# Performance work log

Hardware: AMD Instinct MI355X
Metric: run time of the kernel (lower is better)

The kernel has to match this reference:

```python
import jax, jax.numpy as jnp
import numpy as np

NQ, NT, D = 8192, 8192, 128
EC, EQ, ET = 262144, 262144, 262144


def seg_softmax(logits, seg, num):
    # numerically stable segment softmax over a 1-D logits vector
    m = jax.ops.segment_max(logits, seg, num_segments=num)
    e = jnp.exp(logits - m[seg])
    s = jax.ops.segment_sum(e, seg, num_segments=num)
    return e / s[seg]


def _linear_params(key, din, dout):
    k1, k2 = jax.random.split(key)
    scale = 1.0 / np.sqrt(din)
    W = jax.random.uniform(k1, (din, dout), minval=-scale, maxval=scale, dtype=jnp.float32)
    b = jax.random.uniform(k2, (dout,), minval=-scale, maxval=scale, dtype=jnp.float32)
    return W, b


def setup_inputs():
    key = jax.random.key(0)
    ks = jax.random.split(key, 20)
    inp = {
        'Xq': jax.random.normal(ks[0], (NQ, D), dtype=jnp.float32),
        'edge_index_q': jax.random.randint(ks[1], (2, EQ), 0, NQ),
        'Xt': jax.random.normal(ks[2], (NT, D), dtype=jnp.float32),
        'edge_index_t': jax.random.randint(ks[3], (2, ET), 0, NT),
        'norm_q': jax.random.uniform(ks[4], (NQ, 1), dtype=jnp.float32),
        'norm_t': jax.random.uniform(ks[5], (NT, 1), dtype=jnp.float32),
        'cross_src': jax.random.randint(ks[6], (EC,), 0, NQ),
        'cross_dst': jax.random.randint(ks[7], (EC,), 0, NT),
        'node_mask': jnp.ones((NQ,), dtype=bool),
        'only_run_inter': 0,
    }
    names_dims = [
        ('ac_q', D, D), ('ac_t', D, D), ('vc_q', D, D), ('vc_t', D, D),
        ('mq', 2 * D, D), ('mt', 3 * D, D),
        ('aq', 2 * D, 1), ('vq', 2 * D, D), ('at', 2 * D, 1), ('vt', 2 * D, D),
    ]
    for i, (nm, din, dout) in enumerate(names_dims):
        W, b = _linear_params(ks[8 + i], din, dout)
        inp['W_' + nm] = W
        inp['b_' + nm] = b
    return inp


def reference(Xq, edge_index_q, Xt, edge_index_t, norm_q, norm_t, cross_src, cross_dst,
              node_mask, only_run_inter,
              W_ac_q, b_ac_q, W_ac_t, b_ac_t, W_vc_q, b_vc_q, W_vc_t, b_vc_t,
              W_mq, b_mq, W_mt, b_mt,
              W_aq, b_aq, W_vq, b_vq, W_at, b_at, W_vt, b_vt):
    elu = jax.nn.elu
    nq, nt, d = Xq.shape[0], Xt.shape[0], Xq.shape[1]

    # cross-graph attention logits: per (u, v) pair, dot of transformed features
    Xq_ac = elu(Xq @ W_ac_q + b_ac_q)
    Xt_ac = elu(Xt @ W_ac_t + b_ac_t)
    att_logits = jnp.sum(Xq_ac[cross_src] * Xt_ac[cross_dst], axis=-1)  # [EC]

    # t2q: aggregate target values into query nodes (faithful to original: values gathered by u indices)
    Xt_vc = elu(Xt @ W_vc_t + b_vc_t)
    att_u = seg_softmax(att_logits, cross_src, nq)[:, None]
    Xt2q = jax.ops.segment_sum(att_u * Xt_vc[cross_src], cross_src, num_segments=nq)
    Xq_merged = jnp.concatenate([Xq, Xt2q], axis=1) @ W_mq + b_mq

    # q2t: aggregate query values into target nodes, plus global query summary Q
    Xq_vc = elu(Xq @ W_vc_q + b_vc_q)
    att_v = seg_softmax(att_logits, cross_dst, nt)[:, None]
    Xq2t = jax.ops.segment_sum(att_v * Xq_vc[cross_src], cross_dst, num_segments=nt)
    Q = jnp.broadcast_to(jnp.mean(Xq, axis=0, keepdims=True), (nt, d))
    Xt_merged = jnp.concatenate([Xt, Xq2t, Q], axis=1) @ W_mt + b_mt

    if only_run_inter:
        return Xq_merged, Xt_merged

    # intra-graph edge-wise gather -> MLP -> softmax-scatter message passing
    msg_t = jnp.concatenate([Xt_merged[edge_index_t[0]], Xt_merged[edge_index_t[1]]], axis=1)  # [ET, 2D]
    a_t = seg_softmax((msg_t @ W_at + b_at)[:, 0], edge_index_t[1], nt)[:, None]
    Xt_out = jax.ops.segment_sum(a_t * (msg_t @ W_vt + b_vt), edge_index_t[1], num_segments=nt)

    msg_q = jnp.concatenate([Xq_merged[edge_index_q[0]], Xq_merged[edge_index_q[1]]], axis=1)  # [EQ, 2D]
    a_q = seg_softmax((msg_q @ W_aq + b_aq)[:, 0], edge_index_q[1], nq)[:, None]
    Xq_out = jax.ops.segment_sum(a_q * (msg_q @ W_vq + b_vq), edge_index_q[1], num_segments=nq)

    return Xq_out, Xt_out
```

## Files before the change

### kernel.cpp

```cpp
#include <hip/hip_runtime.h>
#include <math.h>


#define NBIN 8192
#define NB   128

typedef _Float16 h2f __attribute__((ext_vector_type(2)));
typedef __attribute__((ext_vector_type(8))) short short8;
typedef __attribute__((ext_vector_type(4))) float f32x4;

__device__ __forceinline__ float elu1(float x) { return x > 0.f ? x : __expf(x) - 1.f; }

__device__ __forceinline__ unsigned short f2bf(float x) {
    unsigned u = __float_as_uint(x);
    u += 0x7FFF + ((u >> 16) & 1);
    return (unsigned short)(u >> 16);
}
__device__ __forceinline__ float bflo(unsigned u) { return __uint_as_float(u << 16); }
__device__ __forceinline__ float bfhi(unsigned u) { return __uint_as_float(u & 0xFFFF0000u); }
__device__ __forceinline__ unsigned short f2h(float x) {
    return __builtin_bit_cast(unsigned short, (_Float16)x);
}

__device__ __forceinline__ float dot8_f16(const uint4 a, const uint4 b, float d) {
#if __has_builtin(__builtin_amdgcn_fdot2)
    d = __builtin_amdgcn_fdot2(__builtin_bit_cast(h2f, a.x), __builtin_bit_cast(h2f, b.x), d, false);
    d = __builtin_amdgcn_fdot2(__builtin_bit_cast(h2f, a.y), __builtin_bit_cast(h2f, b.y), d, false);
    d = __builtin_amdgcn_fdot2(__builtin_bit_cast(h2f, a.z), __builtin_bit_cast(h2f, b.z), d, false);
    d = __builtin_amdgcn_fdot2(__builtin_bit_cast(h2f, a.w), __builtin_bit_cast(h2f, b.w), d, false);
#else
    const unsigned ua[4] = { a.x, a.y, a.z, a.w };
    const unsigned ub[4] = { b.x, b.y, b.z, b.w };
    #pragma unroll
    for (int t = 0; t < 4; ++t) {
        const h2f ha = __builtin_bit_cast(h2f, ua[t]);
        const h2f hb = __builtin_bit_cast(h2f, ub[t]);
        d = fmaf((float)ha.x, (float)hb.x, d);
        d = fmaf((float)ha.y, (float)hb.y, d);
    }
#endif
    return d;
}

__device__ void wprep_body(const float* __restrict__ S, unsigned short* __restrict__ Wf)
{
    const int lane = threadIdx.x & 63;
    const int fg = threadIdx.x >> 6;
    const int l15 = lane & 15, quad = lane >> 4;
    for (int f = fg; f < 32; f += 4) {
        const int nt = f >> 2, kc = f & 3;
        const int n = nt * 16 + l15;
        const int ks = kc * 32 + quad * 8;
        unsigned short pk[8];
        #pragma unroll
        for (int jj = 0; jj < 8; ++jj)
            pk[jj] = f2bf(S[(size_t)(ks + jj) * 128 + n]);
        uint4 v;
        v.x = (unsigned)pk[0] | ((unsigned)pk[1] << 16);
        v.y = (unsigned)pk[2] | ((unsigned)pk[3] << 16);
        v.z = (unsigned)pk[4] | ((unsigned)pk[5] << 16);
        v.w = (unsigned)pk[6] | ((unsigned)pk[7] << 16);
        *(uint4*)&Wf[((size_t)f * 64 + lane) * 8] = v;
    }
}

__device__ void hist_body(int k, int a, int* h,
                          const int* __restrict__ cs, const int* __restrict__ cd,
                          const int* __restrict__ et1, const int* __restrict__ eq1,
                          int* __restrict__ mask_src, unsigned short* __restrict__ partial,
                          int EC, int ET, int EQ)
{
    const int tid = threadIdx.x;
    const int* idxs[3] = { cd, et1, eq1 };
    const int Es[3] = { EC, ET, EQ };
    for (int b = tid; b < NBIN; b += 256) h[b] = 0;
    __syncthreads();
    const int E = Es[a];
    const int per = (E + NB - 1) / NB;
    const int lo = k * per;
    const int hi = min(E, lo + per);
    const int* idx = idxs[a];
    for (int e = lo + tid; e < hi; e += 256) {
        atomicAdd(&h[idx[e]], 1);
        if (a == 0) mask_src[cs[e]] = 1;
    }
    __syncthreads();
    unsigned short* P = partial + ((size_t)a * NB + k) * NBIN;
    for (int b = tid; b < NBIN; b += 256) P[b] = (unsigned short)h[b];
}

__device__ void colsum_body(int bx, const float* __restrict__ X, float* __restrict__ sum)
{
    const int c = threadIdx.x & 127;
    const int half = threadIdx.x >> 7;
    float s = 0.f;
    #pragma unroll 8
    for (int j = 0; j < 64; ++j) {
        const int r = bx * 128 + half + 2 * j;
        s += X[(size_t)r * 128 + c];
    }
    atomicAdd(&sum[c], s);
}

struct WSrcs { const float* s[12]; };

__global__ __launch_bounds__(256) void prep(
    const int* cs, const int* cd, const int* et1, const int* eq1,
    int* mask_src, unsigned short* partial, int EC, int ET, int EQ,
    WSrcs ws, unsigned short* wt, const float* Xq, float* Qsum)
{
    __shared__ int smem_h[NBIN];
    int b = blockIdx.x;
    if (b < 3 * NB) {
        hist_body(b % NB, b / NB, smem_h, cs, cd, et1, eq1, mask_src, partial, EC, ET, EQ);
    } else if ((b -= 3 * NB) < 12) {
        wprep_body(ws.s[b], wt + (size_t)b * 16384);
    } else {
        colsum_body(b - 12, Xq, Qsum);
    }
}

struct MJob {
    const float* A0; const float* A1; const int* rowmask1;
    const unsigned short* W[2][2];
    const float* bias0; const float* bias1;
    float* C0; float* C1;
    unsigned short* Cb0; unsigned short* Cb1;
    unsigned short* Ch0; unsigned short* Ch1;
    const float* gvw; float* gvo;
    int act;
};

__global__ __launch_bounds__(256) void gemm_mfma(MJob j0, MJob j1)
{
    const MJob j = blockIdx.z ? j1 : j0;
    const int c0 = blockIdx.y * 64;
    const int r0 = blockIdx.x * 64;
    __shared__ unsigned short AhL[64][136];
    __shared__ unsigned short AlL[64][136];
    const int tid = threadIdx.x;
    const int wv = tid >> 6, lane = tid & 63;
    const int l15 = lane & 15, quad = lane >> 4;

    f32x4 acc[2][4] = {};

    for (int pass = 0; pass < 2; ++pass) {
        const float* A = pass ? j.A1 : j.A0;
        if (!A) break;
        {
            const int row = tid >> 2, kq = (tid & 3) * 32;
            const int gr = r0 + row;
            const bool zero = pass && j.rowmask1 && (j.rowmask1[gr] == 0);
            const float* src = A + (size_t)gr * 128 + kq;
            #pragma unroll
            for (int c = 0; c < 32; c += 4) {
                float4 v = *(const float4*)(src + c);
                if (zero) v = make_float4(0.f, 0.f, 0.f, 0.f);
                const float xv[4] = { v.x, v.y, v.z, v.w };
                unsigned short hh[4], ll[4];
                #pragma unroll
                for (int u = 0; u < 4; ++u) {
                    const unsigned short hb = f2bf(xv[u]);
                    hh[u] = hb;
                    ll[u] = f2bf(xv[u] - __uint_as_float((unsigned)hb << 16));
                }
                uint2 ph, pl;
                ph.x = (unsigned)hh[0] | ((unsigned)hh[1] << 16);
                ph.y = (unsigned)hh[2] | ((unsigned)hh[3] << 16);
                pl.x = (unsigned)ll[0] | ((unsigned)ll[1] << 16);
                pl.y = (unsigned)ll[2] | ((unsigned)ll[3] << 16);
                *(uint2*)&AhL[row][kq + c] = ph;
                *(uint2*)&AlL[row][kq + c] = pl;
            }
        }
        __syncthreads();
        #pragma unroll
        for (int kc = 0; kc < 4; ++kc) {
            const short8 ah = *(const short8*)&AhL[wv * 16 + l15][kc * 32 + quad * 8];
            const short8 al = *(const short8*)&AlL[wv * 16 + l15][kc * 32 + quad * 8];
            #pragma unroll
            for (int out = 0; out < 2; ++out) {
                const unsigned short* Wf = j.W[pass][out];
                if (!Wf) continue;
                #pragma unroll
                for (int ni = 0; ni < 4; ++ni) {
                    const short8 bh = *(const short8*)&Wf[
                        ((size_t)(((c0 >> 4) + ni) * 4 + kc) * 64 + lane) * 8];
                    acc[out][ni] = __builtin_amdgcn_mfma_f32_16x16x32_bf16(ah, bh, acc[out][ni], 0, 0, 0);
                    acc[out][ni] = __builtin_amdgcn_mfma_f32_16x16x32_bf16(al, bh, acc[out][ni], 0, 0, 0);
                }
            }
        }
        __syncthreads();
    }

    #pragma unroll
    for (int out = 0; out < 2; ++out) {
        if (!j.W[0][out] && !j.W[1][out]) continue;
        const float* bias = out ? j.bias1 : j.bias0;
        float* C = out ? j.C1 : j.C0;
        unsigned short* Cb = out ? j.Cb1 : j.Cb0;
        unsigned short* Ch = out ? j.Ch1 : j.Ch0;
        const int dogv = (j.gvw != nullptr) && (out == 0);
        float p[4] = {};
        #pragma unroll
        for (int ni = 0; ni < 4; ++ni) {
            const int col = c0 + ni * 16 + l15;
            const float bvl = bias ? bias[col] : 0.f;
            const float gw = dogv ? j.gvw[col] : 0.f;
            #pragma unroll
            for (int reg = 0; reg < 4; ++reg) {
                float o = acc[out][ni][reg] + bvl;
                if (j.act) o = elu1(o);
                const int row = r0 + wv * 16 + quad * 4 + reg;
                if (C) C[(size_t)row * 128 + col] = o;
                else if (Cb) Cb[(size_t)row * 128 + col] = f2bf(o);
                else Ch[(size_t)row * 128 + col] = f2h(o);
                p[reg] = fmaf(o, gw, p[reg]);
            }
        }
        if (dogv) {
            #pragma unroll
            for (int reg = 0; reg < 4; ++reg) {
                float v = p[reg];
                v += __shfl_xor(v, 1, 64); v += __shfl_xor(v, 2, 64);
                v += __shfl_xor(v, 4, 64); v += __shfl_xor(v, 8, 64);
                if (l15 == 0)
                    atomicAdd(j.gvo + r0 + wv * 16 + quad * 4 + reg, v);
            }
        }
    }
}

__global__ void binprefix_kernel(unsigned short* __restrict__ partial, int* __restrict__ cnt)
{
    const int bin = blockIdx.x * 256 + threadIdx.x;
    const int a = blockIdx.y;
    unsigned short* P = partial + (size_t)a * NB * NBIN;
    int s = 0;
    #pragma unroll 4
    for (int k = 0; k < NB; ++k) {
        const int p = P[(size_t)k * NBIN + bin];
        P[(size_t)k * NBIN + bin] = (unsigned short)s;
        s += p;
    }
    cnt[a * NBIN + bin] = s;
}

__global__ __launch_bounds__(1024) void scan3_kernel(const int* __restrict__ cnt, int* __restrict__ offs)
{
    const int b = blockIdx.x;
    const int* c = cnt + (size_t)b * NBIN;
    int* o = offs + (size_t)b * (NBIN + 1);
    __shared__ int sums[1024];
    const int tid = threadIdx.x;
    int loc[8]; int s = 0;
    #pragma unroll
    for (int j = 0; j < 8; ++j) { loc[j] = s; s += c[tid * 8 + j]; }
    sums[tid] = s;
    __syncthreads();
    for (int off = 1; off < 1024; off <<= 1) {
        int v = 0;
        if (tid >= off) v = sums[tid - off];
        __syncthreads();
        sums[tid] += v;
        __syncthreads();
    }
    const int ex = tid ? sums[tid - 1] : 0;
    #pragma unroll
    for (int j = 0; j < 8; ++j) o[tid * 8 + j] = ex + loc[j];
    if (tid == 1023) o[NBIN] = sums[1023];
}

__device__ void scatter_body(int k, int a, int* cur,
    const int* __restrict__ cs, const int* __restrict__ cd,
    const int* __restrict__ et0, const int* __restrict__ et1,
    const int* __restrict__ eq0, const int* __restrict__ eq1,
    const unsigned short* __restrict__ partial, const int* __restrict__ offs,
    int* __restrict__ ids_cd, int* __restrict__ ids_t, int* __restrict__ ids_q,
    int EC, int ET, int EQ)
{
    const int tid = threadIdx.x;
    const int Es[3] = { EC, ET, EQ };
    const int* seg[3] = { cd, et1, eq1 };
    const int* pay[3] = { cs, et0, eq0 };
    int* dst[3] = { ids_cd, ids_t, ids_q };
    const unsigned short* P = partial + ((size_t)a * NB + k) * NBIN;
    const int* off = offs + (size_t)a * (NBIN + 1);
    for (int b = tid; b < NBIN; b += 256) cur[b] = off[b] + (int)P[b];
    __syncthreads();
    const int E = Es[a];
    const int per = (E + NB - 1) / NB;
    const int lo = k * per;
    const int hi = min(E, lo + per);
    const int* sg = seg[a]; const int* pl = pay[a]; int* dd = dst[a];
    for (int e = lo + tid; e < hi; e += 256) {
        const int pos = atomicAdd(&cur[sg[e]], 1);
        dd[pos] = pl[e];
    }
}

__device__ void mt_extra_body(float* red,
    const float* __restrict__ Qsum, const float* __restrict__ Wmt,
    const float* __restrict__ bmt, float* __restrict__ outv, int M)
{
    const int c = threadIdx.x & 127, h = threadIdx.x >> 7;
    const float inv = 1.0f / (float)M;
    float acc = 0.f;
    #pragma unroll 4
    for (int k = h * 64; k < h * 64 + 64; ++k)
        acc = fmaf(Qsum[k] * inv, Wmt[(size_t)(256 + k) * 128 + c], acc);
    red[h * 128 + c] = acc;
    __syncthreads();
    if (h == 0) outv[c] = bmt[c] + red[c] + red[128 + c];
}

__global__ __launch_bounds__(256) void stage3(
    const int* cs, const int* cd,
    const int* et0, const int* et1, const int* eq0, const int* eq1,
    const unsigned short* partial, const int* offs,
    int* ids_cd, int* ids_t, int* ids_q, int EC, int ET, int EQ,
    const float* Qsum, const float* Wmt, const float* bmt, float* mte, int M)
{
    __shared__ __align__(16) char smem[32768];
    const int b = blockIdx.x;
    if (b < 3 * NB)
        scatter_body(b % NB, b / NB, (int*)smem, cs, cd, et0, et1, eq0, eq1,
                     partial, offs, ids_cd, ids_t, ids_q, EC, ET, EQ);
    else
        mt_extra_body((float*)smem, Qsum, Wmt, bmt, mte, M);
}

__device__ __forceinline__ void gather_chunk_bf(
    const unsigned int* __restrict__ rows, int myid, float wv, int rem,
    int half, int cl, float4& acc)
{
    const int npairs = (rem + 1) >> 1;
    int j = 0;
    for (; j + 4 <= npairs; j += 4) {
        const int e0 = 2 * j + half, e1 = e0 + 2, e2 = e0 + 4, e3 = e0 + 6;
        const int s0 = __shfl(myid, e0, 64); const float w0 = __shfl(wv, e0, 64);
        const int s1 = __shfl(myid, e1, 64); const float w1 = __shfl(wv, e1, 64);
        const int s2 = __shfl(myid, e2, 64); const float w2 = __shfl(wv, e2, 64);
        const int s3 = __shfl(myid, e3, 64); const float w3 = __shfl(wv, e3, 64);
        const uint2 v0 = *(const uint2*)(rows + (size_t)s0 * 64 + cl * 2);
        const uint2 v1 = *(const uint2*)(rows + (size_t)s1 * 64 + cl * 2);
        const uint2 v2 = *(const uint2*)(rows + (size_t)s2 * 64 + cl * 2);
        const uint2 v3 = *(const uint2*)(rows + (size_t)s3 * 64 + cl * 2);
        acc.x = fmaf(w0, bflo(v0.x), acc.x); acc.y = fmaf(w0, bfhi(v0.x), acc.y);
        acc.z = fmaf(w0, bflo(v0.y), acc.z); acc.w = fmaf(w0, bfhi(v0.y), acc.w);
        acc.x = fmaf(w1, bflo(v1.x), acc.x); acc.y = fmaf(w1, bfhi(v1.x), acc.y);
        acc.z = fmaf(w1, bflo(v1.y), acc.z); acc.w = fmaf(w1, bfhi(v1.y), acc.w);
        acc.x = fmaf(w2, bflo(v2.x), acc.x); acc.y = fmaf(w2, bfhi(v2.x), acc.y);
        acc.z = fmaf(w2, bflo(v2.y), acc.z); acc.w = fmaf(w2, bfhi(v2.y), acc.w);
        acc.x = fmaf(w3, bflo(v3.x), acc.x); acc.y = fmaf(w3, bfhi(v3.x), acc.y);
        acc.z = fmaf(w3, bflo(v3.y), acc.z); acc.w = fmaf(w3, bfhi(v3.y), acc.w);
    }
    for (; j < npairs; ++j) {
        const int e = 2 * j + half;
        const int sv = __shfl(myid, e, 64); const float we = __shfl(wv, e, 64);
        const uint2 v = *(const uint2*)(rows + (size_t)sv * 64 + cl * 2);
        acc.x = fmaf(we, bflo(v.x), acc.x); acc.y = fmaf(we, bfhi(v.x), acc.y);
        acc.z = fmaf(we, bflo(v.y), acc.z); acc.w = fmaf(we, bfhi(v.y), acc.w);
    }
}

__global__ __launch_bounds__(256) void seg_agg_intra(
    const int* ot, const int* it, const float* nlt, const unsigned int* rt,
    const float* xt, const float* ebt, float* outt,
    const int* oq, const int* iq, const float* nlq, const unsigned int* rq,
    const float* xq, const float* ebq, float* outq, int nseg)
{
    const int* offs; const int* ids; const float* nl; const unsigned int* rows;
    const float* extra; const float* eb; float* out;
    if (blockIdx.y == 0) { offs = ot; ids = it; nl = nlt; rows = rt; extra = xt; eb = ebt; out = outt; }
    else                 { offs = oq; ids = iq; nl = nlq; rows = rq; extra = xq; eb = ebq; out = outq; }
    const int wid = (int)((blockIdx.x * blockDim.x + threadIdx.x) >> 6);
    const int lane = threadIdx.x & 63;
    if (wid >= nseg) return;
    const int lo = offs[wid], hi = offs[wid + 1];
    if (lo == hi) {
        *(float2*)(out + (size_t)wid * 128 + lane * 2) = make_float2(0.f, 0.f);
        return;
    }
    const int half = lane >> 5, cl = lane & 31;
    float m = -3.4e38f, s = 0.f;
    float4 acc = make_float4(0.f, 0.f, 0.f, 0.f);
    for (int base = lo; base < hi; base += 64) {
        const int rem = min(64, hi - base);
        int myid = 0; float l = -3.4e38f;
        if (lane < rem) { myid = ids[base + lane]; l = nl[myid]; }
        float mc = l;
        #pragma unroll
        for (int t = 32; t; t >>= 1) mc = fmaxf(mc, __shfl_xor(mc, t, 64));
        const float nm = fmaxf(m, mc);
        const float alpha = __expf(m - nm);
        const float wv = (lane < rem) ? __expf(l - nm) : 0.f;
        s = s * alpha + wv;
        acc.x *= alpha; acc.y *= alpha; acc.z *= alpha; acc.w *= alpha;
        m = nm;
        gather_chunk_bf(rows, myid, wv, rem, half, cl, acc);
    }
    #pragma unroll
    for (int t = 32; t; t >>= 1) s += __shfl_xor(s, t, 64);
    acc.x += __shfl_xor(acc.x, 32, 64); acc.y += __shfl_xor(acc.y, 32, 64);
    acc.z += __shfl_xor(acc.z, 32, 64); acc.w += __shfl_xor(acc.w, 32, 64);
    if (half == 0) {
        const float inv = 1.f / s;
        const float4 xv = *(const float4*)(extra + (size_t)wid * 128 + cl * 4);
        const float4 bv = *(const float4*)(eb + cl * 4);
        float4 o;
        o.x = fmaf(acc.x, inv, xv.x + bv.x);
        o.y = fmaf(acc.y, inv, xv.y + bv.y);
        o.z = fmaf(acc.z, inv, xv.z + bv.z);
        o.w = fmaf(acc.w, inv, xv.w + bv.w);
        *(float4*)(out + (size_t)wid * 128 + cl * 4) = o;
    }
}

__global__ __launch_bounds__(256) void seg_agg_cross(
    const int* __restrict__ offs, const int* __restrict__ ids,
    const unsigned int* __restrict__ Aqh, const unsigned int* __restrict__ Ath,
    const unsigned int* __restrict__ Vqb, float* __restrict__ out, int nseg)
{
    __shared__ unsigned int atrowh[4][64];
    const int w = threadIdx.x >> 6;
    const int lane = threadIdx.x & 63;
    const int wid = blockIdx.x * 4 + w;
    if (wid >= nseg) return;
    const int lo = offs[wid], hi = offs[wid + 1];
    if (lo == hi) {
        *(float2*)(out + (size_t)wid * 128 + lane * 2) = make_float2(0.f, 0.f);
        return;
    }
    atrowh[w][lane] = Ath[(size_t)wid * 64 + lane];
    __threadfence_block();

    const int half = lane >> 5, cl = lane & 31;
    float m = -3.4e38f, s = 0.f;
    float4 acc = make_float4(0.f, 0.f, 0.f, 0.f);
    for (int base = lo; base < hi; base += 64) {
        const int rem = min(64, hi - base);
        int myid = 0; float d = -3.4e38f;
        if (lane < rem) {
            myid = ids[base + lane];
            const unsigned int* ar = Aqh + (size_t)myid * 64;
            d = 0.f;
            #pragma unroll
            for (int k = 0; k < 64; k += 4)
                d = dot8_f16(*(const uint4*)(ar + k), *(const uint4*)&atrowh[w][k], d);
        }
        float mc = d;
        #pragma unroll
        for (int t = 32; t; t >>= 1) mc = fmaxf(mc, __shfl_xor(mc, t, 64));
        const float nm = fmaxf(m, mc);
        const float alpha = __expf(m - nm);
        const float wv = (lane < rem) ? __expf(d - nm) : 0.f;
        s = s * alpha + wv;
        acc.x *= alpha; acc.y *= alpha; acc.z *= alpha; acc.w *= alpha;
        m = nm;
        gather_chunk_bf(Vqb, myid, wv, rem, half, cl, acc);
    }
    #pragma unroll
    for (int t = 32; t; t >>= 1) s += __shfl_xor(s, t, 64);
    acc.x += __shfl_xor(acc.x, 32, 64); acc.y += __shfl_xor(acc.y, 32, 64);
    acc.z += __shfl_xor(acc.z, 32, 64); acc.w += __shfl_xor(acc.w, 32, 64);
    if (half == 0) {
        const float inv = 1.f / s;
        float4 o;
        o.x = acc.x * inv; o.y = acc.y * inv; o.z = acc.z * inv; o.w = acc.w * inv;
        *(float4*)(out + (size_t)wid * 128 + cl * 4) = o;
    }
}

extern "C" void kernel_launch(void* const* d_in, const int* in_sizes, int n_in,
                              void* d_out, int out_size, void* d_ws, size_t ws_size,
                              hipStream_t stream)
{
    const float* Xq    = (const float*)d_in[0];
    const int*   eqidx = (const int*)d_in[1];
    const float* Xt    = (const float*)d_in[2];
    const int*   etidx = (const int*)d_in[3];
    const int*   cs    = (const int*)d_in[6];
    const int*   cd    = (const int*)d_in[7];
    const float* W_ac_q = (const float*)d_in[10]; const float* b_ac_q = (const float*)d_in[11];
    const float* W_ac_t = (const float*)d_in[12]; const float* b_ac_t = (const float*)d_in[13];
    const float* W_vc_q = (const float*)d_in[14]; const float* b_vc_q = (const float*)d_in[15];
    const float* W_vc_t = (const float*)d_in[16]; const float* b_vc_t = (const float*)d_in[17];
    const float* W_mq   = (const float*)d_in[18]; const float* b_mq   = (const float*)d_in[19];
    const float* W_mt   = (const float*)d_in[20]; const float* b_mt   = (const float*)d_in[21];
    const float* W_aq   = (const float*)d_in[22];
    const float* W_vq   = (const float*)d_in[24]; const float* b_vq   = (const float*)d_in[25];
    const float* W_at   = (const float*)d_in[26];
    const float* W_vt   = (const float*)d_in[28]; const float* b_vt   = (const float*)d_in[29];

    const int NQ = in_sizes[0] / 128;
    const int EQ = in_sizes[1] / 2;
    const int NT = in_sizes[2] / 128;
    const int ET = in_sizes[3] / 2;
    const int EC = in_sizes[6];

    const int* eq0 = eqidx;  const int* eq1 = eqidx + EQ;
    const int* et0 = etidx;  const int* et1 = etidx + ET;

    float* base = (float*)d_ws;
    size_t off = 0;
    auto alloc = [&](size_t n) { float* p = base + off; off += n; return p; };
    float* N1 = alloc((size_t)NT * 128);
    float* N2 = alloc((size_t)NQ * 128);
    float* N3 = alloc((size_t)NT * 128);
    float* N4 = alloc((size_t)NT * 128);
    unsigned int* A0h = (unsigned int*)alloc((size_t)NQ * 64);
    unsigned int* A1h = (unsigned int*)alloc((size_t)NT * 64);
    unsigned short* B0 = (unsigned short*)alloc((size_t)NQ * 64);
    unsigned short* B1 = (unsigned short*)alloc((size_t)NT * 64);
    unsigned short* B2 = (unsigned short*)alloc((size_t)NQ * 64);
    unsigned short* WT = (unsigned short*)alloc((size_t)12 * 16384 / 2);
    float* mte  = alloc(128);
    float* st0v = alloc((size_t)NT);
    float* sq0v = alloc((size_t)NQ);
    int* mask_src = (int*)alloc((size_t)NQ);
    float* Qsum   = alloc(128);
    const size_t zero_bytes = ((size_t)NT + NQ + NQ + 128) * 4;
    int* cnt  = (int*)alloc((size_t)3 * NBIN);
    int* offs = (int*)alloc((size_t)3 * (NBIN + 1));
    unsigned short* partial = (unsigned short*)alloc((size_t)3 * NB * NBIN / 2);
    int* ids_cd = (int*)alloc((size_t)EC);
    int* ids_t  = (int*)alloc((size_t)ET);
    int* ids_q  = (int*)alloc((size_t)EQ);

    float* Xq_out = (float*)d_out;
    float* Xt_out = (float*)d_out + (size_t)NQ * 128;

    const int* offs_cd = offs;
    const int* offs_t  = offs + (NBIN + 1);
    const int* offs_q  = offs + 2 * (NBIN + 1);

    auto WTp = [&](int i) { return (const unsigned short*)(WT + (size_t)i * 16384); };

    hipMemsetAsync(st0v, 0, zero_bytes, stream);

    WSrcs ws;
    ws.s[0] = W_ac_q; ws.s[1] = W_vc_q; ws.s[2] = W_ac_t; ws.s[3] = W_vc_t;
    ws.s[4] = W_mq;   ws.s[5] = W_mq + 16384;
    ws.s[6] = W_mt;   ws.s[7] = W_mt + 16384;
    ws.s[8] = W_vt;   ws.s[9] = W_vt + 16384;
    ws.s[10] = W_vq;  ws.s[11] = W_vq + 16384;
    prep<<<3 * NB + 12 + NQ / 128, 256, 0, stream>>>(
        cs, cd, et1, eq1, mask_src, partial, EC, ET, EQ, ws, WT, Xq, Qsum);

    binprefix_kernel<<<dim3(NBIN / 256, 3), 256, 0, stream>>>(partial, cnt);
    scan3_kernel<<<3, 1024, 0, stream>>>(cnt, offs);

    stage3<<<3 * NB + 1, 256, 0, stream>>>(cs, cd, et0, et1, eq0, eq1, partial, offs,
                                           ids_cd, ids_t, ids_q, EC, ET, EQ,
                                           Qsum, W_mt, b_mt, mte, NQ);

    const dim3 gg(NQ / 64, 2, 2);

    MJob jq{}, jt{};
    jq.A0 = Xq; jq.W[0][0] = WTp(0); jq.W[0][1] = WTp(1);
    jq.bias0 = b_ac_q; jq.bias1 = b_vc_q;
    jq.Ch0 = (unsigned short*)A0h; jq.Cb1 = B0; jq.act = 1;
    jt.A0 = Xt; jt.W[0][0] = WTp(2); jt.W[0][1] = WTp(3);
    jt.bias0 = b_ac_t; jt.bias1 = b_vc_t;
    jt.Ch0 = (unsigned short*)A1h; jt.C1 = N3; jt.act = 1;
    gemm_mfma<<<gg, 256, 0, stream>>>(jq, jt);

    seg_agg_cross<<<(NT + 3) / 4, 256, 0, stream>>>(offs_cd, ids_cd, A0h, A1h,
                                                    (const unsigned int*)B0, N4, NT);

    MJob mq{}, mt{};
    mq.A0 = Xq; mq.W[0][0] = WTp(4);
    mq.A1 = N3; mq.W[1][0] = WTp(5); mq.rowmask1 = mask_src;
    mq.bias0 = b_mq; mq.C0 = N2; mq.gvw = W_aq; mq.gvo = sq0v; mq.act = 0;
    mt.A0 = Xt; mt.W[0][0] = WTp(6);
    mt.A1 = N4; mt.W[1][0] = WTp(7);
    mt.bias0 = mte; mt.C0 = N1; mt.gvw = W_at; mt.gvo = st0v; mt.act = 0;
    gemm_mfma<<<gg, 256, 0, stream>>>(mq, mt);

    MJob ut{}, uq{};
    ut.A0 = N1; ut.W[0][0] = WTp(8); ut.W[0][1] = WTp(9);
    ut.Cb0 = B1; ut.C1 = Xt_out; ut.act = 0;
    uq.A0 = N2; uq.W[0][0] = WTp(10); uq.W[0][1] = WTp(11);
    uq.Cb0 = B2; uq.C1 = Xq_out; uq.act = 0;
    gemm_mfma<<<gg, 256, 0, stream>>>(ut, uq);

    seg_agg_intra<<<dim3((NT + 3) / 4, 2), 256, 0, stream>>>(
        offs_t, ids_t, st0v, (const unsigned int*)B1, Xt_out, b_vt, Xt_out,
        offs_q, ids_q, sq0v, (const unsigned int*)B2, Xq_out, b_vq, Xq_out, NT);
}
```

Baseline: 235.0 us.

## Fuse preprocessing kernels and replace atomics with partial buffers to cut launches

Removes the memset, binprefix and scan3 launches. The bin prefix now runs alongside the first GEMM in a combined stage2 kernel, and each scatter block rebuilds the exclusive scan itself. The atomic column sum, the atomic GEMV outputs and the mask_src writes are replaced by deterministic partial buffers that later kernels reduce. The source mask is now a histogram of cross_src, and NB is halved. The cross aggregation splits the dot product across half-waves, processing 32 edges per iteration instead of 64. The cost is redundant scan work in every scatter block and extra reduction passes.

Result: slower. 282.2 us (+20.1%).

```diff
diff --git a/kernel.cpp b/kernel.cpp
--- a/kernel.cpp
+++ b/kernel.cpp
@@ -3,7 +3,8 @@
 
 
 #define NBIN 8192
-#define NB   128
+#define NB   64
+#define NARR 4
 
 typedef _Float16 h2f __attribute__((ext_vector_type(2)));
 typedef __attribute__((ext_vector_type(8))) short short8;
@@ -67,56 +68,51 @@
 __device__ void hist_body(int k, int a, int* h,
                           const int* __restrict__ cs, const int* __restrict__ cd,
                           const int* __restrict__ et1, const int* __restrict__ eq1,
-                          int* __restrict__ mask_src, unsigned short* __restrict__ partial,
-                          int EC, int ET, int EQ)
+                          unsigned short* __restrict__ partial, int EC, int ET, int EQ)
 {
     const int tid = threadIdx.x;
-    const int* idxs[3] = { cd, et1, eq1 };
-    const int Es[3] = { EC, ET, EQ };
+    const int* idxs[NARR] = { cd, et1, eq1, cs };
+    const int Es[NARR] = { EC, ET, EQ, EC };
     for (int b = tid; b < NBIN; b += 256) h[b] = 0;
     __syncthreads();
     const int E = Es[a];
     const int per = (E + NB - 1) / NB;
-    const int lo = k * per;
-    const int hi = min(E, lo + per);
+    const int lo = k * per, hi = min(E, lo + per);
     const int* idx = idxs[a];
-    for (int e = lo + tid; e < hi; e += 256) {
-        atomicAdd(&h[idx[e]], 1);
-        if (a == 0) mask_src[cs[e]] = 1;
-    }
+    for (int e = lo + tid; e < hi; e += 256) atomicAdd(&h[idx[e]], 1);
     __syncthreads();
     unsigned short* P = partial + ((size_t)a * NB + k) * NBIN;
     for (int b = tid; b < NBIN; b += 256) P[b] = (unsigned short)h[b];
 }
 
-__device__ void colsum_body(int bx, const float* __restrict__ X, float* __restrict__ sum)
-{
-    const int c = threadIdx.x & 127;
-    const int half = threadIdx.x >> 7;
+__device__ void colsum_body(int bx, const float* __restrict__ X, float* sh,
+                            float* __restrict__ Qpart)
+{
+    const int c = threadIdx.x & 127, half = threadIdx.x >> 7;
     float s = 0.f;
     #pragma unroll 8
-    for (int j = 0; j < 64; ++j) {
-        const int r = bx * 128 + half + 2 * j;
-        s += X[(size_t)r * 128 + c];
-    }
-    atomicAdd(&sum[c], s);
+    for (int j = 0; j < 64; ++j)
+        s += X[(size_t)(bx * 128 + half + 2 * j) * 128 + c];
+    sh[threadIdx.x] = s;
+    __syncthreads();
+    if (half == 0) Qpart[bx * 128 + c] = sh[c] + sh[128 + c];
 }
 
 struct WSrcs { const float* s[12]; };
 
 __global__ __launch_bounds__(256) void prep(
     const int* cs, const int* cd, const int* et1, const int* eq1,
-    int* mask_src, unsigned short* partial, int EC, int ET, int EQ,
-    WSrcs ws, unsigned short* wt, const float* Xq, float* Qsum)
-{
-    __shared__ int smem_h[NBIN];
+    unsigned short* partial, int EC, int ET, int EQ,
+    WSrcs ws, unsigned short* wt, const float* Xq, float* Qpart)
+{
+    __shared__ __align__(16) int smem_h[NBIN];
     int b = blockIdx.x;
-    if (b < 3 * NB) {
-        hist_body(b % NB, b / NB, smem_h, cs, cd, et1, eq1, mask_src, partial, EC, ET, EQ);
-    } else if ((b -= 3 * NB) < 12) {
+    if (b < NARR * NB) {
+        hist_body(b % NB, b / NB, smem_h, cs, cd, et1, eq1, partial, EC, ET, EQ);
+    } else if ((b -= NARR * NB) < 12) {
         wprep_body(ws.s[b], wt + (size_t)b * 16384);
     } else {
-        colsum_body(b - 12, Xq, Qsum);
+        colsum_body(b - 12, Xq, (float*)smem_h, Qpart);
     }
 }
 
@@ -131,14 +127,14 @@
     int act;
 };
 
-__global__ __launch_bounds__(256) void gemm_mfma(MJob j0, MJob j1)
-{
-    const MJob j = blockIdx.z ? j1 : j0;
-    const int c0 = blockIdx.y * 64;
-    const int r0 = blockIdx.x * 64;
-    __shared__ unsigned short AhL[64][136];
-    __shared__ unsigned short AlL[64][136];
-    const int tid = threadIdx.x;
+#define GEMM_SMEM (2 * 64 * 136 * 2)
+
+__device__ void gemm_body(const MJob& j, int bx, int by, char* smem, int tid)
+{
+    const int c0 = by * 64;
+    const int r0 = bx * 64;
+    unsigned short (*AhL)[136] = (unsigned short(*)[136])smem;
+    unsigned short (*AlL)[136] = (unsigned short(*)[136])(smem + 64 * 136 * 2);
     const int wv = tid >> 6, lane = tid & 63;
     const int l15 = lane & 15, quad = lane >> 4;
 
@@ -226,16 +222,29 @@
                 v += __shfl_xor(v, 1, 64); v += __shfl_xor(v, 2, 64);
                 v += __shfl_xor(v, 4, 64); v += __shfl_xor(v, 8, 64);
                 if (l15 == 0)
-                    atomicAdd(j.gvo + r0 + wv * 16 + quad * 4 + reg, v);
+                    j.gvo[(c0 >> 6) * NBIN + r0 + wv * 16 + quad * 4 + reg] = v;
             }
         }
     }
 }
 
-__global__ void binprefix_kernel(unsigned short* __restrict__ partial, int* __restrict__ cnt)
-{
-    const int bin = blockIdx.x * 256 + threadIdx.x;
-    const int a = blockIdx.y;
+__global__ __launch_bounds__(256) void gemm_mfma(
+    MJob j0, MJob j1, int ngx,
+    const float* p0, const float* p1, float* o0, float* o1)
+{
+    __shared__ __align__(16) char smem[GEMM_SMEM];
+    if ((int)blockIdx.x == ngx) {
+        const int g = ((blockIdx.y << 1) | blockIdx.z) * 256 + threadIdx.x;
+        for (int i = g; i < NBIN; i += 1024) o0[i] = p0[i] + p0[NBIN + i];
+        for (int i = g; i < NBIN; i += 1024) o1[i] = p1[i] + p1[NBIN + i];
+        return;
+    }
+    gemm_body(blockIdx.z ? j1 : j0, blockIdx.x, blockIdx.y, smem, threadIdx.x);
+}
+
+__device__ void binprefix_body(int bin, int a, unsigned short* __restrict__ partial,
+                               int* __restrict__ cnt)
+{
     unsigned short* P = partial + (size_t)a * NB * NBIN;
     int s = 0;
     #pragma unroll 4
@@ -247,52 +256,63 @@
     cnt[a * NBIN + bin] = s;
 }
 
-__global__ __launch_bounds__(1024) void scan3_kernel(const int* __restrict__ cnt, int* __restrict__ offs)
-{
-    const int b = blockIdx.x;
-    const int* c = cnt + (size_t)b * NBIN;
-    int* o = offs + (size_t)b * (NBIN + 1);
-    __shared__ int sums[1024];
-    const int tid = threadIdx.x;
-    int loc[8]; int s = 0;
-    #pragma unroll
-    for (int j = 0; j < 8; ++j) { loc[j] = s; s += c[tid * 8 + j]; }
-    sums[tid] = s;
-    __syncthreads();
-    for (int off = 1; off < 1024; off <<= 1) {
-        int v = 0;
-        if (tid >= off) v = sums[tid - off];
-        __syncthreads();
-        sums[tid] += v;
-        __syncthreads();
-    }
-    const int ex = tid ? sums[tid - 1] : 0;
-    #pragma unroll
-    for (int j = 0; j < 8; ++j) o[tid * 8 + j] = ex + loc[j];
-    if (tid == 1023) o[NBIN] = sums[1023];
-}
-
-__device__ void scatter_body(int k, int a, int* cur,
+__global__ __launch_bounds__(256) void stage2(
+    MJob j0, MJob j1, int ngx, unsigned short* partial, int* cnt)
+{
+    __shared__ __align__(16) char smem[GEMM_SMEM];
+    int b = blockIdx.x;
+    const int NG = ngx * 4;
+    if (b < NG) {
+        const int bx = b % ngx, r = b / ngx;
+        gemm_body((r >> 1) ? j1 : j0, bx, r & 1, smem, threadIdx.x);
+    } else {
+        b -= NG;
+        binprefix_body((b & 31) * 256 + threadIdx.x, b >> 5, partial, cnt);
+    }
+}
+
+__device__ void scatter_body(int k, int a, char* smemraw,
     const int* __restrict__ cs, const int* __restrict__ cd,
     const int* __restrict__ et0, const int* __restrict__ et1,
     const int* __restrict__ eq0, const int* __restrict__ eq1,
-    const unsigned short* __restrict__ partial, const int* __restrict__ offs,
+    const unsigned short* __restrict__ partial, const int* __restrict__ cnt,
+    int* __restrict__ offs,
     int* __restrict__ ids_cd, int* __restrict__ ids_t, int* __restrict__ ids_q,
     int EC, int ET, int EQ)
 {
+    int* cur = (int*)smemraw;
+    int* sums = cur + NBIN;
     const int tid = threadIdx.x;
     const int Es[3] = { EC, ET, EQ };
     const int* seg[3] = { cd, et1, eq1 };
     const int* pay[3] = { cs, et0, eq0 };
     int* dst[3] = { ids_cd, ids_t, ids_q };
+    const int* c = cnt + (size_t)a * NBIN;
     const unsigned short* P = partial + ((size_t)a * NB + k) * NBIN;
-    const int* off = offs + (size_t)a * (NBIN + 1);
-    for (int b = tid; b < NBIN; b += 256) cur[b] = off[b] + (int)P[b];
+    int* offo = offs + (size_t)a * (NBIN + 1);
+    const int base = tid * 32;
+    int s = 0;
+    #pragma unroll 8
+    for (int i = 0; i < 32; ++i) s += c[base + i];
+    sums[tid] = s;
     __syncthreads();
-    const int E = Es[a];
-    const int per = (E + NB - 1) / NB;
-    const int lo = k * per;
-    const int hi = min(E, lo + per);
+    for (int off = 1; off < 256; off <<= 1) {
+        int v = (tid >= off) ? sums[tid - off] : 0;
+        __syncthreads();
+        sums[tid] += v;
+        __syncthreads();
+    }
+    int run = tid ? sums[tid - 1] : 0;
+    for (int i = 0; i < 32; ++i) {
+        const int bin = base + i;
+        cur[bin] = run + (int)P[bin];
+        if (k == 0) offo[bin] = run;
+        run += c[bin];
+    }
+    if (k == 0 && tid == 0) offo[NBIN] = Es[a];
+    __syncthreads();
+    const int per = (Es[a] + NB - 1) / NB;
+    const int lo = k * per, hi = min(Es[a], lo + per);
     const int* sg = seg[a]; const int* pl = pay[a]; int* dd = dst[a];
     for (int e = lo + tid; e < hi; e += 256) {
         const int pos = atomicAdd(&cur[sg[e]], 1);
@@ -300,35 +320,44 @@
     }
 }
 
-__device__ void mt_extra_body(float* red,
-    const float* __restrict__ Qsum, const float* __restrict__ Wmt,
-    const float* __restrict__ bmt, float* __restrict__ outv, int M)
-{
-    const int c = threadIdx.x & 127, h = threadIdx.x >> 7;
+__device__ void mt_extra_body(char* smemraw, const float* __restrict__ Qpart,
+    const float* __restrict__ Wmt, const float* __restrict__ bmt,
+    float* __restrict__ outv, int M)
+{
+    float* red = (float*)smemraw;
+    float* Qs = red + 256;
+    const int tid = threadIdx.x;
+    if (tid < 128) {
+        float q = 0.f;
+        for (int b = 0; b < 64; ++b) q += Qpart[b * 128 + tid];
+        Qs[tid] = q;
+    }
+    __syncthreads();
+    const int cc = tid & 127, h = tid >> 7;
     const float inv = 1.0f / (float)M;
     float acc = 0.f;
     #pragma unroll 4
-    for (int k = h * 64; k < h * 64 + 64; ++k)
-        acc = fmaf(Qsum[k] * inv, Wmt[(size_t)(256 + k) * 128 + c], acc);
-    red[h * 128 + c] = acc;
+    for (int kk = h * 64; kk < h * 64 + 64; ++kk)
+        acc = fmaf(Qs[kk] * inv, Wmt[(size_t)(256 + kk) * 128 + cc], acc);
+    red[tid] = acc;
     __syncthreads();
-    if (h == 0) outv[c] = bmt[c] + red[c] + red[128 + c];
+    if (h == 0) outv[cc] = bmt[cc] + red[cc] + red[128 + cc];
 }
 
 __global__ __launch_bounds__(256) void stage3(
     const int* cs, const int* cd,
     const int* et0, const int* et1, const int* eq0, const int* eq1,
-    const unsigned short* partial, const int* offs,
+    const unsigned short* partial, const int* cnt, int* offs,
     int* ids_cd, int* ids_t, int* ids_q, int EC, int ET, int EQ,
-    const float* Qsum, const float* Wmt, const float* bmt, float* mte, int M)
-{
-    __shared__ __align__(16) char smem[32768];
+    const float* Qpart, const float* Wmt, const float* bmt, float* mte, int M)
+{
+    __shared__ __align__(16) char smem[NBIN * 4 + 256 * 4];
     const int b = blockIdx.x;
     if (b < 3 * NB)
-        scatter_body(b % NB, b / NB, (int*)smem, cs, cd, et0, et1, eq0, eq1,
-                     partial, offs, ids_cd, ids_t, ids_q, EC, ET, EQ);
+        scatter_body(b % NB, b / NB, smem, cs, cd, et0, et1, eq0, eq1,
+                     partial, cnt, offs, ids_cd, ids_t, ids_q, EC, ET, EQ);
     else
-        mt_extra_body((float*)smem, Qsum, Wmt, bmt, mte, M);
+        mt_extra_body(smem, Qpart, Wmt, bmt, mte, M);
 }
 
 __device__ __forceinline__ void gather_chunk_bf(
@@ -436,36 +465,38 @@
     atrowh[w][lane] = Ath[(size_t)wid * 64 + lane];
     __threadfence_block();
 
-    const int half = lane >> 5, cl = lane & 31;
+    const int eh = lane & 31, dh = lane >> 5, cl = lane & 31;
     float m = -3.4e38f, s = 0.f;
     float4 acc = make_float4(0.f, 0.f, 0.f, 0.f);
-    for (int base = lo; base < hi; base += 64) {
-        const int rem = min(64, hi - base);
+    for (int base = lo; base < hi; base += 32) {
+        const int rem = min(32, hi - base);
         int myid = 0; float d = -3.4e38f;
-        if (lane < rem) {
-            myid = ids[base + lane];
-            const unsigned int* ar = Aqh + (size_t)myid * 64;
+        if (eh < rem) {
+            myid = ids[base + eh];
+            const unsigned int* ar = Aqh + (size_t)myid * 64 + dh * 32;
+            const unsigned int* br = &atrowh[w][dh * 32];
             d = 0.f;
             #pragma unroll
-            for (int k = 0; k < 64; k += 4)
-                d = dot8_f16(*(const uint4*)(ar + k), *(const uint4*)&atrowh[w][k], d);
+            for (int k = 0; k < 32; k += 4)
+                d = dot8_f16(*(const uint4*)(ar + k), *(const uint4*)(br + k), d);
         }
+        d += __shfl_xor(d, 32, 64);
         float mc = d;
         #pragma unroll
-        for (int t = 32; t; t >>= 1) mc = fmaxf(mc, __shfl_xor(mc, t, 64));
+        for (int t = 16; t; t >>= 1) mc = fmaxf(mc, __shfl_xor(mc, t, 64));
         const float nm = fmaxf(m, mc);
         const float alpha = __expf(m - nm);
-        const float wv = (lane < rem) ? __expf(d - nm) : 0.f;
+        const float wv = (dh == 0 && eh < rem) ? __expf(d - nm) : 0.f;
         s = s * alpha + wv;
         acc.x *= alpha; acc.y *= alpha; acc.z *= alpha; acc.w *= alpha;
         m = nm;
-        gather_chunk_bf(Vqb, myid, wv, rem, half, cl, acc);
+        gather_chunk_bf(Vqb, myid, wv, rem, dh, cl, acc);
     }
     #pragma unroll
     for (int t = 32; t; t >>= 1) s += __shfl_xor(s, t, 64);
     acc.x += __shfl_xor(acc.x, 32, 64); acc.y += __shfl_xor(acc.y, 32, 64);
     acc.z += __shfl_xor(acc.z, 32, 64); acc.w += __shfl_xor(acc.w, 32, 64);
-    if (half == 0) {
+    if (dh == 0) {
         const float inv = 1.f / s;
         float4 o;
         o.x = acc.x * inv; o.y = acc.y * inv; o.z = acc.z * inv; o.w = acc.w * inv;
@@ -517,14 +548,14 @@
     unsigned short* B2 = (unsigned short*)alloc((size_t)NQ * 64);
     unsigned short* WT = (unsigned short*)alloc((size_t)12 * 16384 / 2);
     float* mte  = alloc(128);
-    float* st0v = alloc((size_t)NT);
-    float* sq0v = alloc((size_t)NQ);
-    int* mask_src = (int*)alloc((size_t)NQ);
-    float* Qsum   = alloc(128);
-    const size_t zero_bytes = ((size_t)NT + NQ + NQ + 128) * 4;
-    int* cnt  = (int*)alloc((size_t)3 * NBIN);
+    float* st0p = alloc((size_t)2 * NBIN);
+    float* sq0p = alloc((size_t)2 * NBIN);
+    float* st0v = alloc((size_t)NBIN);
+    float* sq0v = alloc((size_t)NBIN);
+    float* Qpart = alloc((size_t)64 * 128);
+    int* cnt  = (int*)alloc((size_t)NARR * NBIN);
     int* offs = (int*)alloc((size_t)3 * (NBIN + 1));
-    unsigned short* partial = (unsigned short*)alloc((size_t)3 * NB * NBIN / 2);
+    unsigned short* partial = (unsigned short*)alloc((size_t)NARR * NB * NBIN / 2);
     int* ids_cd = (int*)alloc((size_t)EC);
     int* ids_t  = (int*)alloc((size_t)ET);
     int* ids_q  = (int*)alloc((size_t)EQ);
@@ -535,10 +566,9 @@
     const int* offs_cd = offs;
     const int* offs_t  = offs + (NBIN + 1);
     const int* offs_q  = offs + 2 * (NBIN + 1);
+    const int* cnt_src = cnt + 3 * NBIN;
 
     auto WTp = [&](int i) { return (const unsigned short*)(WT + (size_t)i * 16384); };
-
-    hipMemsetAsync(st0v, 0, zero_bytes, stream);
 
     WSrcs ws;
     ws.s[0] = W_ac_q; ws.s[1] = W_vc_q; ws.s[2] = W_ac_t; ws.s[3] = W_vc_t;
@@ -546,17 +576,10 @@
     ws.s[6] = W_mt;   ws.s[7] = W_mt + 16384;
     ws.s[8] = W_vt;   ws.s[9] = W_vt + 16384;
     ws.s[10] = W_vq;  ws.s[11] = W_vq + 16384;
-    prep<<<3 * NB + 12 + NQ / 128, 256, 0, stream>>>(
-        cs, cd, et1, eq1, mask_src, partial, EC, ET, EQ, ws, WT, Xq, Qsum);
-
-    binprefix_kernel<<<dim3(NBIN / 256, 3), 256, 0, stream>>>(partial, cnt);
-    scan3_kernel<<<3, 1024, 0, stream>>>(cnt, offs);
-
-    stage3<<<3 * NB + 1, 256, 0, stream>>>(cs, cd, et0, et1, eq0, eq1, partial, offs,
-                                           ids_cd, ids_t, ids_q, EC, ET, EQ,
-                                           Qsum, W_mt, b_mt, mte, NQ);
-
-    const dim3 gg(NQ / 64, 2, 2);
+    prep<<<NARR * NB + 12 + NQ / 128, 256, 0, stream>>>(
+        cs, cd, et1, eq1, partial, EC, ET, EQ, ws, WT, Xq, Qpart);
+
+    const int ngx = NQ / 64;
 
     MJob jq{}, jt{};
     jq.A0 = Xq; jq.W[0][0] = WTp(0); jq.W[0][1] = WTp(1);
@@ -565,26 +588,31 @@
     jt.A0 = Xt; jt.W[0][0] = WTp(2); jt.W[0][1] = WTp(3);
     jt.bias0 = b_ac_t; jt.bias1 = b_vc_t;
     jt.Ch0 = (unsigned short*)A1h; jt.C1 = N3; jt.act = 1;
-    gemm_mfma<<<gg, 256, 0, stream>>>(jq, jt);
+    stage2<<<ngx * 4 + NARR * (NBIN / 256), 256, 0, stream>>>(jq, jt, ngx, partial, cnt);
+
+    stage3<<<3 * NB + 1, 256, 0, stream>>>(cs, cd, et0, et1, eq0, eq1,
+                                           partial, cnt, offs,
+                                           ids_cd, ids_t, ids_q, EC, ET, EQ,
+                                           Qpart, W_mt, b_mt, mte, NQ);
 
     seg_agg_cross<<<(NT + 3) / 4, 256, 0, stream>>>(offs_cd, ids_cd, A0h, A1h,
                                                     (const unsigned int*)B0, N4, NT);
 
     MJob mq{}, mt{};
     mq.A0 = Xq; mq.W[0][0] = WTp(4);
-    mq.A1 = N3; mq.W[1][0] = WTp(5); mq.rowmask1 = mask_src;
-    mq.bias0 = b_mq; mq.C0 = N2; mq.gvw = W_aq; mq.gvo = sq0v; mq.act = 0;
+    mq.A1 = N3; mq.W[1][0] = WTp(5); mq.rowmask1 = cnt_src;
+    mq.bias0 = b_mq; mq.C0 = N2; mq.gvw = W_aq; mq.gvo = sq0p; mq.act = 0;
     mt.A0 = Xt; mt.W[0][0] = WTp(6);
     mt.A1 = N4; mt.W[1][0] = WTp(7);
-    mt.bias0 = mte; mt.C0 = N1; mt.gvw = W_at; mt.gvo = st0v; mt.act = 0;
-    gemm_mfma<<<gg, 256, 0, stream>>>(mq, mt);
+    mt.bias0 = mte; mt.C0 = N1; mt.gvw = W_at; mt.gvo = st0p; mt.act = 0;
+    gemm_mfma<<<dim3(ngx, 2, 2), 256, 0, stream>>>(mq, mt, -1, nullptr, nullptr, nullptr, nullptr);
 
     MJob ut{}, uq{};
     ut.A0 = N1; ut.W[0][0] = WTp(8); ut.W[0][1] = WTp(9);
     ut.Cb0 = B1; ut.C1 = Xt_out; ut.act = 0;
     uq.A0 = N2; uq.W[0][0] = WTp(10); uq.W[0][1] = WTp(11);
     uq.Cb0 = B2; uq.C1 = Xq_out; uq.act = 0;
-    gemm_mfma<<<gg, 256, 0, stream>>>(ut, uq);
+    gemm_mfma<<<dim3(ngx + 1, 2, 2), 256, 0, stream>>>(ut, uq, ngx, st0p, sq0p, st0v, sq0v);
 
     seg_agg_intra<<<dim3((NT + 3) / 4, 2), 256, 0, stream>>>(
         offs_t, ids_t, st0v, (const unsigned int*)B1, Xt_out, b_vt, Xt_out,
```
